# Performance work log

Hardware: AMD Instinct MI355X
Metric: run time of the kernel (lower is better)

The kernel has to match this reference:

```python
import jax, jax.numpy as jnp
import numpy as np

B, N, IN_C, OUT_C = 32, 1024, 64, 128
ALPHA = 0.2  # LeakyReLU negative slope
NEG_INF = -1e16


def setup_inputs() -> dict:
    key = jax.random.key(0)
    k1, k2, k3, k4, k5 = jax.random.split(key, 5)
    inputs = jax.random.normal(k1, (B, N, IN_C), dtype=jnp.float32)
    # dense 0/1 adjacency mask
    graph = jax.random.randint(k2, (N, N), 0, 2).astype(jnp.float32)
    # torch nn.Linear weight layout: [out_c, in_c]
    W = jax.random.normal(k3, (OUT_C, IN_C), dtype=jnp.float32)
    b = jax.random.normal(k4, (OUT_C,), dtype=jnp.float32)
    a = jax.random.normal(k5, (2 * OUT_C, 1), dtype=jnp.float32)
    return {"inputs": inputs, "graph": graph, "W": W, "b": b, "a": a}


def reference(inputs, graph, W, b, a):
    # h = W(inputs): [B, N, D]
    h = jnp.einsum('bnt,dt->bnd', inputs, W)
    # cat([h_i, h_j]) @ a  ==  h_i @ a1 + h_j @ a2  (decomposed, no [B,N,N,2D] tensor)
    a1 = a[:OUT_C, 0]   # [D]
    a2 = a[OUT_C:, 0]   # [D]
    s1 = jnp.einsum('bnd,d->bn', h, a1)  # score contribution of node i
    s2 = jnp.einsum('bnd,d->bn', h, a2)  # score contribution of node j
    e = s1[:, :, None] + s2[:, None, :]  # [B, N, N]
    e = jnp.where(e > 0, e, ALPHA * e)   # LeakyReLU
    e = e * graph                        # zero out non-edges
    # torch masked_fill_(eq(outputs, 0), -1e16)
    e = jnp.where(e == 0.0, NEG_INF, e)
    attention = jax.nn.softmax(e, axis=2)  # [B, N, N]
    out = jnp.einsum('bij,bjd->bid', attention, h) + b  # [B, N, D]
    return out
```

## Files before the change

kernel.cpp:

```cpp
#include <hip/hip_runtime.h>
#include <hip/hip_bf16.h>

#define ALPHA 0.2f

typedef unsigned short ushort_t;
typedef unsigned int   uint_t;
typedef unsigned short ushort8 __attribute__((ext_vector_type(8)));
typedef unsigned short ushortv4 __attribute__((ext_vector_type(4)));
typedef float f32x4 __attribute__((ext_vector_type(4)));
typedef __bf16 bf16x8 __attribute__((ext_vector_type(8)));

__device__ __forceinline__ ushort_t f2bf(float f) {
  unsigned u = __float_as_uint(f);
  u += 0x7fffu + ((u >> 16) & 1u);
  return (ushort_t)(u >> 16);
}
__device__ __forceinline__ float bf2f(ushort_t b) {
  return __uint_as_float((unsigned)b << 16);
}

__global__ __launch_bounds__(256) void gat_pack_kernel(
    const float* __restrict__ graph, const float* __restrict__ W,
    const float* __restrict__ avec, uint_t* __restrict__ gmask,
    float* __restrict__ u)
{
  const int row = blockIdx.x, t = threadIdx.x;
  __shared__ uint_t nibs[256];
  float4 g = ((const float4*)(graph + (size_t)row * 1024))[t];
  uint_t nib = (g.x != 0.f ? 1u : 0u) | (g.y != 0.f ? 2u : 0u) |
               (g.z != 0.f ? 4u : 0u) | (g.w != 0.f ? 8u : 0u);
  nibs[t] = nib;
  __syncthreads();
  if (t < 32) {
    uint_t wd = 0;
#pragma unroll
    for (int k = 0; k < 8; ++k) wd |= nibs[t * 8 + k] << (4 * k);
    gmask[(size_t)row * 32 + t] = wd;
  }
  if (row == 0 && t < 128) {
    const int k  = t & 63;
    const int ao = (t >> 6) * 128;
    float a0 = 0.f, a1 = 0.f, a2 = 0.f, a3 = 0.f;
    for (int d = 0; d < 128; d += 4) {
      a0 = fmaf(avec[ao + d + 0], W[(d + 0) * 64 + k], a0);
      a1 = fmaf(avec[ao + d + 1], W[(d + 1) * 64 + k], a1);
      a2 = fmaf(avec[ao + d + 2], W[(d + 2) * 64 + k], a2);
      a3 = fmaf(avec[ao + d + 3], W[(d + 3) * 64 + k], a3);
    }
    u[t] = (a0 + a1) + (a2 + a3);
  }
}

__global__ __launch_bounds__(256) void gat_h_kernel(
    const float* __restrict__ inp, const float* __restrict__ W,
    const float* __restrict__ uvec, ushort_t* __restrict__ hT,
    float* __restrict__ s1, float* __restrict__ s2)
{
  const int b  = blockIdx.x >> 4;
  const int n0 = (blockIdx.x & 15) << 6;
  const int t  = threadIdx.x;
  const int d  = t & 127;
  const int nh = t >> 7;

  __shared__ float    x_lds[64][68];
  __shared__ float    u_lds[128];
  __shared__ ushort_t h_tile[128][72];

  float wreg[64];
  {
    const float4* wrow = (const float4*)(W + d * 64);
#pragma unroll
    for (int k = 0; k < 16; ++k) {
      float4 v = wrow[k];
      wreg[4*k+0] = v.x; wreg[4*k+1] = v.y; wreg[4*k+2] = v.z; wreg[4*k+3] = v.w;
    }
  }
  if (t < 128) u_lds[t] = uvec[t];

  {
    const float4* xsrc = (const float4*)(inp + ((size_t)b * 1024 + n0) * 64);
#pragma unroll
    for (int k = 0; k < 4; ++k) {
      const int g = k * 256 + t;
      const int n = g >> 4, c = g & 15;
      *(float4*)&x_lds[n][c * 4] = xsrc[g];
    }
  }
  __syncthreads();

  for (int r = 0; r < 32; ++r) {
    const int n = nh * 32 + r;
    const float* xr = &x_lds[n][0];
    float ax = 0.f, ay = 0.f, az = 0.f, aw = 0.f;
#pragma unroll
    for (int k = 0; k < 16; ++k) {
      float4 xv = *(const float4*)&xr[4 * k];
      ax = fmaf(wreg[4*k+0], xv.x, ax);
      ay = fmaf(wreg[4*k+1], xv.y, ay);
      az = fmaf(wreg[4*k+2], xv.z, az);
      aw = fmaf(wreg[4*k+3], xv.w, aw);
    }
    h_tile[d][n] = f2bf((ax + ay) + (az + aw));
  }

  if (t < 128) {
    const int n = t & 63, which = t >> 6;
    const float* xr = &x_lds[n][0];
    const float* uu = &u_lds[which * 64];
    float a0 = 0.f, a1 = 0.f, a2 = 0.f, a3 = 0.f;
#pragma unroll
    for (int k = 0; k < 16; ++k) {
      float4 xv = *(const float4*)&xr[4 * k];
      a0 = fmaf(xv.x, uu[4*k+0], a0);
      a1 = fmaf(xv.y, uu[4*k+1], a1);
      a2 = fmaf(xv.z, uu[4*k+2], a2);
      a3 = fmaf(xv.w, uu[4*k+3], a3);
    }
    const float sv = (a0 + a1) + (a2 + a3);
    if (which == 0) s1[(size_t)b * 1024 + n0 + n] = sv;
    else            s2[(size_t)b * 1024 + n0 + n] = sv;
  }
  __syncthreads();

#pragma unroll
  for (int it = 0; it < 4; ++it) {
    const int d2 = it * 32 + (t >> 3);
    const int ch = (t & 7) * 8;
    ushort8 v = *(const ushort8*)&h_tile[d2][ch];
    *(ushort8*)(hT + ((size_t)b * 128 + d2) * 1024 + n0 + ch) = v;
  }
}

__global__ __launch_bounds__(256) void gat_attn_kernel(
    const uint_t* __restrict__ gmask, const ushort_t* __restrict__ hT,
    const float* __restrict__ s1g, const float* __restrict__ s2g,
    const float* __restrict__ bias, float* __restrict__ out)
{
  const int ic = blockIdx.x;
  const int b  = blockIdx.y;
  const int i0 = ic << 5;
  const int t  = threadIdx.x;
  const int w  = t >> 6;
  const int l  = t & 63;

  __shared__ float    s2_lds[1024];
  __shared__ uint_t   mask_lds[32][33];
  __shared__ ushort_t p_lds[2][32][40];
  __shared__ ushort_t ht_lds[2][128][40];
  __shared__ float    red_part[32][8];
  __shared__ float    red_row[32];

  {
    const float4* src = (const float4*)(s2g + (size_t)b * 1024);
    ((float4*)s2_lds)[t] = src[t];
  }
  {
    const uint4 mv = ((const uint4*)(gmask + (size_t)(i0 + (t >> 3)) * 32))[t & 7];
    const int mr = t >> 3, mc = (t & 7) * 4;
    mask_lds[mr][mc + 0] = mv.x; mask_lds[mr][mc + 1] = mv.y;
    mask_lds[mr][mc + 2] = mv.z; mask_lds[mr][mc + 3] = mv.w;
  }
  const int irow = t >> 3;
  const int jsl  = (t & 7) * 4;
  const int sr   = t >> 2;
  const int sc   = (t & 3) * 8;
  const float s1v = s1g[(size_t)b * 1024 + i0 + irow];
  const ushort_t* htb = hT + (size_t)b * 128 * 1024;
  __syncthreads();

  float mx_local = -1e30f;
  for (int jt = 0; jt < 32; ++jt) {
    const uint_t word = mask_lds[irow][jt];
    float4 sA = *(const float4*)(s2_lds + jt * 32 + jsl);
    if ((word >> (jsl + 0)) & 1u) mx_local = fmaxf(mx_local, sA.x);
    if ((word >> (jsl + 1)) & 1u) mx_local = fmaxf(mx_local, sA.y);
    if ((word >> (jsl + 2)) & 1u) mx_local = fmaxf(mx_local, sA.z);
    if ((word >> (jsl + 3)) & 1u) mx_local = fmaxf(mx_local, sA.w);
  }
  red_part[irow][t & 7] = mx_local;
  __syncthreads();
  if (t < 32) {
    float m = red_part[t][0];
#pragma unroll
    for (int k = 1; k < 8; ++k) m = fmaxf(m, red_part[t][k]);
    red_row[t] = m;
  }
  __syncthreads();
  const float tm = s1v + red_row[irow];
  const float Mi = tm > 0.f ? tm : ALPHA * tm;

  float den_local = 0.f;
  f32x4 c[2][2];
#pragma unroll
  for (int is = 0; is < 2; ++is)
#pragma unroll
    for (int ds = 0; ds < 2; ++ds)
      c[is][ds] = f32x4{0.f, 0.f, 0.f, 0.f};

#define STAGE_COMPUTE(nj, bi, hva, hvb)                                      \
  {                                                                          \
    const uint_t word = mask_lds[irow][nj];                                  \
    const float4 sA = *(const float4*)(s2_lds + (nj) * 32 + jsl);            \
    const float ss[4] = {sA.x, sA.y, sA.z, sA.w};                            \
    ushortv4 pb;                                                             \
    _Pragma("unroll")                                                        \
    for (int e = 0; e < 4; ++e) {                                            \
      float te = s1v + ss[e];                                                \
      float v  = te > 0.f ? te : ALPHA * te;                                 \
      float p  = (((word >> (jsl + e)) & 1u) && v != 0.f)                    \
                     ? __expf(v - Mi) : 0.f;                                 \
      pb[e] = f2bf(p);                                                       \
      den_local += bf2f(pb[e]);                                              \
    }                                                                        \
    *(ushortv4*)&p_lds[bi][irow][jsl] = pb;                                  \
    *(ushort8*)&ht_lds[bi][sr][sc] = (hva);                                  \
    *(ushort8*)&ht_lds[bi][sr + 64][sc] = (hvb);                             \
  }

#define DO_MFMA(bi)                                                          \
  {                                                                          \
    bf16x8 av0 = __builtin_bit_cast(bf16x8,                                  \
        *(const ushort8*)&p_lds[bi][(l & 15)][(l >> 4) * 8]);                \
    bf16x8 av1 = __builtin_bit_cast(bf16x8,                                  \
        *(const ushort8*)&p_lds[bi][16 + (l & 15)][(l >> 4) * 8]);           \
    bf16x8 bv0 = __builtin_bit_cast(bf16x8,                                  \
        *(const ushort8*)&ht_lds[bi][w * 32 + (l & 15)][(l >> 4) * 8]);      \
    bf16x8 bv1 = __builtin_bit_cast(bf16x8,                                  \
        *(const ushort8*)&ht_lds[bi][w * 32 + 16 + (l & 15)][(l >> 4) * 8]); \
    c[0][0] = __builtin_amdgcn_mfma_f32_16x16x32_bf16(av0, bv0, c[0][0], 0, 0, 0); \
    c[1][0] = __builtin_amdgcn_mfma_f32_16x16x32_bf16(av1, bv0, c[1][0], 0, 0, 0); \
    c[0][1] = __builtin_amdgcn_mfma_f32_16x16x32_bf16(av0, bv1, c[0][1], 0, 0, 0); \
    c[1][1] = __builtin_amdgcn_mfma_f32_16x16x32_bf16(av1, bv1, c[1][1], 0, 0, 0); \
  }

  {
    ushort8 hva = *(const ushort8*)(htb + (size_t)sr * 1024 + sc);
    ushort8 hvb = *(const ushort8*)(htb + (size_t)(sr + 64) * 1024 + sc);
    STAGE_COMPUTE(0, 0, hva, hvb);
  }
  __syncthreads();

  int cur = 0;
  for (int jt = 0; jt < 32; ++jt) {
    ushort8 nha, nhb;
    const int nj = jt + 1;
    if (nj < 32) {
      nha = *(const ushort8*)(htb + (size_t)sr * 1024 + nj * 32 + sc);
      nhb = *(const ushort8*)(htb + (size_t)(sr + 64) * 1024 + nj * 32 + sc);
    }
    __builtin_amdgcn_s_setprio(1);
    DO_MFMA(cur);
    __builtin_amdgcn_s_setprio(0);
    if (nj < 32) STAGE_COMPUTE(nj, cur ^ 1, nha, nhb);
    __syncthreads();
    cur ^= 1;
  }

  red_part[irow][t & 7] = den_local;
  __syncthreads();
  if (t < 32) {
    float s = red_part[t][0];
#pragma unroll
    for (int k = 1; k < 8; ++k) s += red_part[t][k];
    red_row[t] = s;
  }
  __syncthreads();

#pragma unroll
  for (int ds = 0; ds < 2; ++ds) {
    const int col = w * 32 + ds * 16 + (l & 15);
    const float bc = bias[col];
#pragma unroll
    for (int is = 0; is < 2; ++is) {
#pragma unroll
      for (int r = 0; r < 4; ++r) {
        const int row = is * 16 + (l >> 4) * 4 + r;
        const float dr = red_row[row];
        const float val = dr > 0.f ? c[is][ds][r] / dr + bc : bc;
        out[((size_t)b * 1024 + i0 + row) * 128 + col] = val;
      }
    }
  }
}

extern "C" void kernel_launch(void* const* d_in, const int* in_sizes, int n_in,
                              void* d_out, int out_size, void* d_ws, size_t ws_size,
                              hipStream_t stream) {
  (void)in_sizes; (void)n_in; (void)out_size; (void)ws_size;
  const float* inp   = (const float*)d_in[0];
  const float* graph = (const float*)d_in[1];
  const float* W     = (const float*)d_in[2];
  const float* bias  = (const float*)d_in[3];
  const float* avec  = (const float*)d_in[4];
  float* out = (float*)d_out;

  char* ws = (char*)d_ws;
  ushort_t* hT = (ushort_t*)ws;
  float* s1    = (float*)(ws + (size_t)8 * 1024 * 1024);
  float* s2    = s1 + 32 * 1024;
  float* u     = s2 + 32 * 1024;
  uint_t* gm   = (uint_t*)(ws + (size_t)8 * 1024 * 1024 + 512 * 1024);

  gat_pack_kernel<<<1024, 256, 0, stream>>>(graph, W, avec, gm, u);
  gat_h_kernel<<<512, 256, 0, stream>>>(inp, W, u, hT, s1, s2);
  gat_attn_kernel<<<dim3(32, 32), 256, 0, stream>>>(gm, hT, s1, s2, bias, out);
}
```

Before: 67.39 us.

## Compute attention probabilities in MFMA register layout, drop LDS staging and barriers

Result: slower. 74.75 us (+10.9%).

```diff
diff --git a/kernel.cpp b/kernel.cpp
--- a/kernel.cpp
+++ b/kernel.cpp
@@ -6,7 +6,7 @@
 typedef unsigned short ushort_t;
 typedef unsigned int   uint_t;
 typedef unsigned short ushort8 __attribute__((ext_vector_type(8)));
-typedef unsigned short ushortv4 __attribute__((ext_vector_type(4)));
+typedef uint_t uintv4 __attribute__((ext_vector_type(4)));
 typedef float f32x4 __attribute__((ext_vector_type(4)));
 typedef __bf16 bf16x8 __attribute__((ext_vector_type(8)));
 
@@ -14,9 +14,6 @@
   unsigned u = __float_as_uint(f);
   u += 0x7fffu + ((u >> 16) & 1u);
   return (ushort_t)(u >> 16);
-}
-__device__ __forceinline__ float bf2f(ushort_t b) {
-  return __uint_as_float((unsigned)b << 16);
 }
 
 __global__ __launch_bounds__(256) void gat_pack_kernel(
@@ -138,144 +135,144 @@
 {
   const int ic = blockIdx.x;
   const int b  = blockIdx.y;
-  const int i0 = ic << 5;
+  const int i0 = ic << 6;
   const int t  = threadIdx.x;
   const int w  = t >> 6;
   const int l  = t & 63;
-
-  __shared__ float    s2_lds[1024];
-  __shared__ uint_t   mask_lds[32][33];
-  __shared__ ushort_t p_lds[2][32][40];
-  __shared__ ushort_t ht_lds[2][128][40];
-  __shared__ float    red_part[32][8];
-  __shared__ float    red_row[32];
-
+  const int ih = w >> 1;
+  const int dh = w & 1;
+  const int rlo = l & 15, rhi = rlo + 16;
+  const int js  = (l >> 4) * 8;
+
+  __shared__ float  s2_lds[1024];
+  __shared__ uint_t mask_lds[64][33];
+  __shared__ float  red_part[64][4];
+  __shared__ float  red_row[64];
+
+  ((float4*)s2_lds)[t] = ((const float4*)(s2g + (size_t)b * 1024))[t];
   {
-    const float4* src = (const float4*)(s2g + (size_t)b * 1024);
-    ((float4*)s2_lds)[t] = src[t];
-  }
+    const uint4* gsrc = (const uint4*)(gmask + (size_t)i0 * 32);
+#pragma unroll
+    for (int k2 = 0; k2 < 2; ++k2) {
+      const int idx = t + k2 * 256;
+      uint4 mv = gsrc[idx];
+      const int mr = idx >> 3, mc = (idx & 7) * 4;
+      mask_lds[mr][mc + 0] = mv.x; mask_lds[mr][mc + 1] = mv.y;
+      mask_lds[mr][mc + 2] = mv.z; mask_lds[mr][mc + 3] = mv.w;
+    }
+  }
+  __syncthreads();
+
   {
-    const uint4 mv = ((const uint4*)(gmask + (size_t)(i0 + (t >> 3)) * 32))[t & 7];
-    const int mr = t >> 3, mc = (t & 7) * 4;
-    mask_lds[mr][mc + 0] = mv.x; mask_lds[mr][mc + 1] = mv.y;
-    mask_lds[mr][mc + 2] = mv.z; mask_lds[mr][mc + 3] = mv.w;
-  }
-  const int irow = t >> 3;
-  const int jsl  = (t & 7) * 4;
-  const int sr   = t >> 2;
-  const int sc   = (t & 3) * 8;
-  const float s1v = s1g[(size_t)b * 1024 + i0 + irow];
-  const ushort_t* htb = hT + (size_t)b * 128 * 1024;
-  __syncthreads();
-
-  float mx_local = -1e30f;
+    const int irow = t >> 2, bo = (t & 3) * 8;
+    float mx = -1e30f;
+    for (int jt = 0; jt < 32; ++jt) {
+      const uint_t wd = mask_lds[irow][jt] >> bo;
+      const float4 sA = *(const float4*)(s2_lds + jt * 32 + bo);
+      const float4 sB = *(const float4*)(s2_lds + jt * 32 + bo + 4);
+      if (wd & 1u)   mx = fmaxf(mx, sA.x);
+      if (wd & 2u)   mx = fmaxf(mx, sA.y);
+      if (wd & 4u)   mx = fmaxf(mx, sA.z);
+      if (wd & 8u)   mx = fmaxf(mx, sA.w);
+      if (wd & 16u)  mx = fmaxf(mx, sB.x);
+      if (wd & 32u)  mx = fmaxf(mx, sB.y);
+      if (wd & 64u)  mx = fmaxf(mx, sB.z);
+      if (wd & 128u) mx = fmaxf(mx, sB.w);
+    }
+    red_part[irow][t & 3] = mx;
+  }
+  __syncthreads();
+  if (t < 64)
+    red_row[t] = fmaxf(fmaxf(red_part[t][0], red_part[t][1]),
+                       fmaxf(red_part[t][2], red_part[t][3]));
+  __syncthreads();
+
+  const int ib = ih * 32;
+  const float s1lo = s1g[(size_t)b * 1024 + i0 + ib + rlo];
+  const float s1hi = s1g[(size_t)b * 1024 + i0 + ib + rhi];
+  const float tl = s1lo + red_row[ib + rlo];
+  const float th = s1hi + red_row[ib + rhi];
+  const float Milo = tl > 0.f ? tl : ALPHA * tl;
+  const float Mihi = th > 0.f ? th : ALPHA * th;
+
+  const ushort_t* hb =
+      hT + (size_t)b * 128 * 1024 + (size_t)(dh * 64 + rlo) * 1024 + js;
+
+  f32x4 c[2][4];
+#pragma unroll
+  for (int is = 0; is < 2; ++is)
+#pragma unroll
+    for (int ds = 0; ds < 4; ++ds) c[is][ds] = f32x4{0.f, 0.f, 0.f, 0.f};
+  float den_lo = 0.f, den_hi = 0.f;
+
+  ushort8 bv[4], nb[4];
+#pragma unroll
+  for (int ds = 0; ds < 4; ++ds)
+    bv[ds] = *(const ushort8*)(hb + (size_t)ds * 16 * 1024);
+
+#pragma unroll 4
   for (int jt = 0; jt < 32; ++jt) {
-    const uint_t word = mask_lds[irow][jt];
-    float4 sA = *(const float4*)(s2_lds + jt * 32 + jsl);
-    if ((word >> (jsl + 0)) & 1u) mx_local = fmaxf(mx_local, sA.x);
-    if ((word >> (jsl + 1)) & 1u) mx_local = fmaxf(mx_local, sA.y);
-    if ((word >> (jsl + 2)) & 1u) mx_local = fmaxf(mx_local, sA.z);
-    if ((word >> (jsl + 3)) & 1u) mx_local = fmaxf(mx_local, sA.w);
-  }
-  red_part[irow][t & 7] = mx_local;
-  __syncthreads();
-  if (t < 32) {
-    float m = red_part[t][0];
-#pragma unroll
-    for (int k = 1; k < 8; ++k) m = fmaxf(m, red_part[t][k]);
-    red_row[t] = m;
-  }
-  __syncthreads();
-  const float tm = s1v + red_row[irow];
-  const float Mi = tm > 0.f ? tm : ALPHA * tm;
-
-  float den_local = 0.f;
-  f32x4 c[2][2];
-#pragma unroll
-  for (int is = 0; is < 2; ++is)
-#pragma unroll
-    for (int ds = 0; ds < 2; ++ds)
-      c[is][ds] = f32x4{0.f, 0.f, 0.f, 0.f};
-
-#define STAGE_COMPUTE(nj, bi, hva, hvb)                                      \
-  {                                                                          \
-    const uint_t word = mask_lds[irow][nj];                                  \
-    const float4 sA = *(const float4*)(s2_lds + (nj) * 32 + jsl);            \
-    const float ss[4] = {sA.x, sA.y, sA.z, sA.w};                            \
-    ushortv4 pb;                                                             \
-    _Pragma("unroll")                                                        \
-    for (int e = 0; e < 4; ++e) {                                            \
-      float te = s1v + ss[e];                                                \
-      float v  = te > 0.f ? te : ALPHA * te;                                 \
-      float p  = (((word >> (jsl + e)) & 1u) && v != 0.f)                    \
-                     ? __expf(v - Mi) : 0.f;                                 \
-      pb[e] = f2bf(p);                                                       \
-      den_local += bf2f(pb[e]);                                              \
-    }                                                                        \
-    *(ushortv4*)&p_lds[bi][irow][jsl] = pb;                                  \
-    *(ushort8*)&ht_lds[bi][sr][sc] = (hva);                                  \
-    *(ushort8*)&ht_lds[bi][sr + 64][sc] = (hvb);                             \
-  }
-
-#define DO_MFMA(bi)                                                          \
-  {                                                                          \
-    bf16x8 av0 = __builtin_bit_cast(bf16x8,                                  \
-        *(const ushort8*)&p_lds[bi][(l & 15)][(l >> 4) * 8]);                \
-    bf16x8 av1 = __builtin_bit_cast(bf16x8,                                  \
-        *(const ushort8*)&p_lds[bi][16 + (l & 15)][(l >> 4) * 8]);           \
-    bf16x8 bv0 = __builtin_bit_cast(bf16x8,                                  \
-        *(const ushort8*)&ht_lds[bi][w * 32 + (l & 15)][(l >> 4) * 8]);      \
-    bf16x8 bv1 = __builtin_bit_cast(bf16x8,                                  \
-        *(const ushort8*)&ht_lds[bi][w * 32 + 16 + (l & 15)][(l >> 4) * 8]); \
-    c[0][0] = __builtin_amdgcn_mfma_f32_16x16x32_bf16(av0, bv0, c[0][0], 0, 0, 0); \
-    c[1][0] = __builtin_amdgcn_mfma_f32_16x16x32_bf16(av1, bv0, c[1][0], 0, 0, 0); \
-    c[0][1] = __builtin_amdgcn_mfma_f32_16x16x32_bf16(av0, bv1, c[0][1], 0, 0, 0); \
-    c[1][1] = __builtin_amdgcn_mfma_f32_16x16x32_bf16(av1, bv1, c[1][1], 0, 0, 0); \
-  }
-
-  {
-    ushort8 hva = *(const ushort8*)(htb + (size_t)sr * 1024 + sc);
-    ushort8 hvb = *(const ushort8*)(htb + (size_t)(sr + 64) * 1024 + sc);
-    STAGE_COMPUTE(0, 0, hva, hvb);
-  }
-  __syncthreads();
-
-  int cur = 0;
-  for (int jt = 0; jt < 32; ++jt) {
-    ushort8 nha, nhb;
-    const int nj = jt + 1;
-    if (nj < 32) {
-      nha = *(const ushort8*)(htb + (size_t)sr * 1024 + nj * 32 + sc);
-      nhb = *(const ushort8*)(htb + (size_t)(sr + 64) * 1024 + nj * 32 + sc);
-    }
-    __builtin_amdgcn_s_setprio(1);
-    DO_MFMA(cur);
-    __builtin_amdgcn_s_setprio(0);
-    if (nj < 32) STAGE_COMPUTE(nj, cur ^ 1, nha, nhb);
-    __syncthreads();
-    cur ^= 1;
-  }
-
-  red_part[irow][t & 7] = den_local;
-  __syncthreads();
-  if (t < 32) {
-    float s = red_part[t][0];
-#pragma unroll
-    for (int k = 1; k < 8; ++k) s += red_part[t][k];
-    red_row[t] = s;
-  }
-  __syncthreads();
-
-#pragma unroll
-  for (int ds = 0; ds < 2; ++ds) {
-    const int col = w * 32 + ds * 16 + (l & 15);
+    const int j0 = jt * 32;
+    const int jn = (jt + 1 < 32) ? j0 + 32 : j0;
+#pragma unroll
+    for (int ds = 0; ds < 4; ++ds)
+      nb[ds] = *(const ushort8*)(hb + (size_t)ds * 16 * 1024 + jn);
+
+    const uint_t wlo = mask_lds[ib + rlo][jt] >> js;
+    const uint_t whi = mask_lds[ib + rhi][jt] >> js;
+    const float4 sA = *(const float4*)(s2_lds + j0 + js);
+    const float4 sB = *(const float4*)(s2_lds + j0 + js + 4);
+    const float sv[8] = {sA.x, sA.y, sA.z, sA.w, sB.x, sB.y, sB.z, sB.w};
+    float plo[8], phi[8];
+#pragma unroll
+    for (int e = 0; e < 8; ++e) {
+      float te = s1lo + sv[e];
+      float v  = fmaxf(te, ALPHA * te);
+      plo[e] = (((wlo >> e) & 1u) && v != 0.f) ? __expf(v - Milo) : 0.f;
+      te = s1hi + sv[e];
+      v  = fmaxf(te, ALPHA * te);
+      phi[e] = (((whi >> e) & 1u) && v != 0.f) ? __expf(v - Mihi) : 0.f;
+    }
+    uint_t pkl[4], pkh[4];
+#pragma unroll
+    for (int q = 0; q < 4; ++q) {
+      asm("v_cvt_pk_bf16_f32 %0, %1, %2"
+          : "=v"(pkl[q]) : "v"(plo[2 * q]), "v"(plo[2 * q + 1]));
+      asm("v_cvt_pk_bf16_f32 %0, %1, %2"
+          : "=v"(pkh[q]) : "v"(phi[2 * q]), "v"(phi[2 * q + 1]));
+      den_lo += __uint_as_float(pkl[q] << 16) +
+                __uint_as_float(pkl[q] & 0xffff0000u);
+      den_hi += __uint_as_float(pkh[q] << 16) +
+                __uint_as_float(pkh[q] & 0xffff0000u);
+    }
+    const bf16x8 av0 =
+        __builtin_bit_cast(bf16x8, (uintv4){pkl[0], pkl[1], pkl[2], pkl[3]});
+    const bf16x8 av1 =
+        __builtin_bit_cast(bf16x8, (uintv4){pkh[0], pkh[1], pkh[2], pkh[3]});
+#pragma unroll
+    for (int ds = 0; ds < 4; ++ds) {
+      const bf16x8 bvv = __builtin_bit_cast(bf16x8, bv[ds]);
+      c[0][ds] = __builtin_amdgcn_mfma_f32_16x16x32_bf16(av0, bvv, c[0][ds], 0, 0, 0);
+      c[1][ds] = __builtin_amdgcn_mfma_f32_16x16x32_bf16(av1, bvv, c[1][ds], 0, 0, 0);
+    }
+#pragma unroll
+    for (int ds = 0; ds < 4; ++ds) bv[ds] = nb[ds];
+  }
+
+  den_lo += __shfl_xor(den_lo, 16); den_lo += __shfl_xor(den_lo, 32);
+  den_hi += __shfl_xor(den_hi, 16); den_hi += __shfl_xor(den_hi, 32);
+
+#pragma unroll
+  for (int ds = 0; ds < 4; ++ds) {
+    const int col = dh * 64 + ds * 16 + rlo;
     const float bc = bias[col];
 #pragma unroll
     for (int is = 0; is < 2; ++is) {
 #pragma unroll
       for (int r = 0; r < 4; ++r) {
-        const int row = is * 16 + (l >> 4) * 4 + r;
-        const float dr = red_row[row];
+        const int row  = ib + is * 16 + (l >> 4) * 4 + r;
+        const int srcl = (l >> 4) * 4 + r;
+        const float dr = is ? __shfl(den_hi, srcl) : __shfl(den_lo, srcl);
         const float val = dr > 0.f ? c[is][ds][r] / dr + bc : bc;
         out[((size_t)b * 1024 + i0 + row) * 128 + col] = val;
       }
@@ -303,5 +300,5 @@
 
   gat_pack_kernel<<<1024, 256, 0, stream>>>(graph, W, avec, gm, u);
   gat_h_kernel<<<512, 256, 0, stream>>>(inp, W, u, hT, s1, s2);
-  gat_attn_kernel<<<dim3(32, 32), 256, 0, stream>>>(gm, hT, s1, s2, bias, out);
-}
+  gat_attn_kernel<<<dim3(16, 32), 256, 0, stream>>>(gm, hT, s1, s2, bias, out);
+}
```
